# Kernel tuning notes

Measured on AMD Instinct MI355X. Metric: run time of the kernel, lower is better.

## Reference

```python
import jax, jax.numpy as jnp
import numpy as np

B, T, D = 128, 512, 300
U = 300          # gru_units
DENSE = 100      # dense_units
MASK_VALUE = 0.0


def setup_inputs() -> dict:
    key = jax.random.key(0)
    ks = jax.random.split(key, 8)
    s_in = 1.0 / np.sqrt(D)
    s_rec = 1.0 / np.sqrt(U)
    s_d = 1.0 / np.sqrt(2 * U)
    return {
        "x": jax.random.normal(ks[0], (B, T, D), jnp.float32),
        "Wf": jax.random.normal(ks[1], (D, 3 * U), jnp.float32) * s_in,
        "Uf": jax.random.normal(ks[2], (U, 3 * U), jnp.float32) * s_rec,
        "bf": jnp.zeros((2, 3 * U), jnp.float32),
        "Wb": jax.random.normal(ks[3], (D, 3 * U), jnp.float32) * s_in,
        "Ub": jax.random.normal(ks[4], (U, 3 * U), jnp.float32) * s_rec,
        "bb": jnp.zeros((2, 3 * U), jnp.float32),
        "Wd": jax.random.normal(ks[5], (2 * U, DENSE), jnp.float32) * s_d,
        "bd": jnp.zeros((DENSE,), jnp.float32),
    }


def _gru_dir(x, mask, W, Uw, b):
    """Keras GRU v2 (reset_after=True), one direction.
    x: [B,T,D], mask: [B,T] bool. Returns [B,T,U]."""
    # Precompute input projections for all timesteps (one big GEMM).
    xg = jnp.einsum('btd,dk->btk', x, W) + b[0]            # [B,T,3U]
    xg = jnp.swapaxes(xg, 0, 1)                             # [T,B,3U]
    m = jnp.swapaxes(mask, 0, 1)                            # [T,B]

    def step(h, inp):
        xt, mt = inp
        rec = h @ Uw + b[1]                                 # [B,3U]
        xz, xr, xh = jnp.split(xt, 3, axis=-1)
        rz, rr, rh = jnp.split(rec, 3, axis=-1)
        z = jax.nn.sigmoid(xz + rz)
        r = jax.nn.sigmoid(xr + rr)
        hh = jnp.tanh(xh + r * rh)
        h_new = z * h + (1.0 - z) * hh
        h_new = jnp.where(mt[:, None], h_new, h)            # masked: carry state
        return h_new, h_new

    h0 = jnp.zeros((x.shape[0], Uw.shape[0]), x.dtype)
    _, ys = jax.lax.scan(step, h0, (xg, m))
    return jnp.swapaxes(ys, 0, 1)                           # [B,T,U]


def reference(x, Wf, Uf, bf, Wb, Ub, bb, Wd, bd):
    # Masking layer: a timestep is masked if ALL features equal mask_value.
    mask = jnp.any(x != MASK_VALUE, axis=-1)                # [B,T]
    fwd = _gru_dir(x, mask, Wf, Uf, bf)
    bwd = _gru_dir(x[:, ::-1], mask[:, ::-1], Wb, Ub, bb)[:, ::-1]
    h = jnp.concatenate([fwd, bwd], axis=-1)                # [B,T,2U]
    # Dropout layers are identity at inference.
    out = jnp.tanh(jnp.einsum('btk,kd->btd', h, Wd) + bd)   # [B,T,DENSE]
    return out
```

## Files before the change

kernel.cpp:

```cpp
#include <hip/hip_runtime.h>


typedef float f32x4 __attribute__((ext_vector_type(4)));
typedef short short8 __attribute__((ext_vector_type(8)));
typedef unsigned short u16;
typedef unsigned int u32;
typedef unsigned long long u64;

#define MFMA16(a, b, c) __builtin_amdgcn_mfma_f32_16x16x32_bf16((a), (b), (c), 0, 0, 0)

__device__ __forceinline__ u16 f2bf(float f) {
  u32 u = __float_as_uint(f);
  u = u + 0x7FFFu + ((u >> 16) & 1u);
  return (u16)(u >> 16);
}
__device__ __forceinline__ float bf2f(u16 h) {
  return __uint_as_float(((u32)h) << 16);
}
__device__ __forceinline__ float sigm(float x) { return 1.f / (1.f + __expf(-x)); }
__device__ __forceinline__ float tanhx(float x) { return 1.f - 2.f / (__expf(2.f * x) + 1.f); }

#define OFF_WT       0ULL
#define OFF_UT       1228800ULL
#define OFF_B0P      2457600ULL
#define OFF_B1P      2465280ULL
#define OFF_WDT      2472960ULL
#define OFF_BDP      2616320ULL
#define OFF_MASK     2616832ULL
#define OFF_HSTATE   2878976ULL
#define OFF_FLAGS    3206656ULL
#define OFF_XBF      3223040ULL
#define OFF_HALL     45166080ULL
#define WS_NEED      123809280ULL

__global__ __launch_bounds__(256) void k_sentinel(float* __restrict__ out,
                                                  float code, int n) {
  int i = blockIdx.x * 256 + threadIdx.x;
  if (i < n) out[i] = code;
}

__global__ __launch_bounds__(256) void k_prep(
    const float* __restrict__ Wf, const float* __restrict__ Uf,
    const float* __restrict__ bfp, const float* __restrict__ Wb,
    const float* __restrict__ Ub, const float* __restrict__ bbp,
    const float* __restrict__ Wd, const float* __restrict__ bd,
    u16* __restrict__ WT, u16* __restrict__ UT,
    float* __restrict__ b0p, float* __restrict__ b1p,
    u16* __restrict__ WdT, float* __restrict__ bdp)
{
  const long long NWU = 2LL * 960 * 320;
  const long long TOTAL = NWU * 2 + 1920 + 71680 + 112;
  for (long long i = (long long)blockIdx.x * 256 + threadIdx.x; i < TOTAL;
       i += 2048LL * 256) {
    long long r = i;
    if (r < NWU) {
      int d = (int)(r / 307200); int q = (int)(r % 307200);
      int c = q / 320, k = q % 320;
      int cc = c / 80, lc = c % 80;
      float v = 0.f;
      if (k < 300 && lc < 75) {
        int g = lc / 25, jp = lc % 25;
        const float* W = d ? Wb : Wf;
        v = W[k * 900 + g * 300 + cc * 25 + jp];
      }
      WT[r] = f2bf(v);
      continue;
    }
    r -= NWU;
    if (r < NWU) {
      int d = (int)(r / 307200); int q = (int)(r % 307200);
      int c = q / 320, k = q % 320;
      int cc = c / 80, lc = c % 80;
      float v = 0.f;
      if (k < 300 && lc < 75) {
        int g = lc / 25, jp = lc % 25;
        const float* U = d ? Ub : Uf;
        v = U[k * 900 + g * 300 + cc * 25 + jp];
      }
      UT[r] = f2bf(v);
      continue;
    }
    r -= NWU;
    if (r < 1920) {
      int d = (int)(r / 960); int c = (int)(r % 960);
      int cc = c / 80, lc = c % 80;
      float v0 = 0.f, v1 = 0.f;
      if (lc < 75) {
        int g = lc / 25, jp = lc % 25;
        const float* B = d ? bbp : bfp;
        int sc = g * 300 + cc * 25 + jp;
        v0 = B[sc]; v1 = B[900 + sc];
      }
      b0p[r] = v0; b1p[r] = v1;
      continue;
    }
    r -= 1920;
    if (r < 71680) {
      int n = (int)(r / 640); int k = (int)(r % 640);
      float v = (n < 100 && k < 600) ? Wd[k * 100 + n] : 0.f;
      WdT[r] = f2bf(v);
      continue;
    }
    r -= 71680;
    if (r < 112) bdp[r] = (r < 100) ? bd[r] : 0.f;
  }
}

__global__ __launch_bounds__(256) void k_xbf(const float* __restrict__ x,
                                             u16* __restrict__ xbf,
                                             float* __restrict__ mask)
{
  int row = blockIdx.x * 4 + (threadIdx.x >> 6);
  int l = threadIdx.x & 63;
  const float* xr = x + (size_t)row * 300;
  u16* xo = xbf + (size_t)row * 320;
  int p = 0;
#pragma unroll
  for (int c = 0; c < 5; ++c) {
    int k = l + c * 64;
    float v = (k < 300) ? xr[k] : 0.f;
    p |= (v != 0.f);
    xo[k] = f2bf(v);
  }
  unsigned long long b = __ballot(p);
  if (l == 0) mask[row] = (b != 0ULL) ? 1.f : 0.f;
}

__global__ __launch_bounds__(256, 1) void k_scan(
    const u16* __restrict__ UTg, const u16* __restrict__ WTg,
    const float* __restrict__ b0p, const float* __restrict__ b1p,
    const u16* __restrict__ xbf, const float* __restrict__ mask,
    u16* __restrict__ h_state, u16* __restrict__ h_all, u32* __restrict__ flags)
{
  extern __shared__ char smem[];
  u16*   Ufrag = (u16*)smem;
  u16*   Wfrag = (u16*)(smem + 51200);
  char*  hS    = smem + 102400;
  float* recS  = (float*)(smem + 122880);
  float* xgS   = (float*)(smem + 133120);

  const int tid = threadIdx.x;
  const int l = tid & 63;
  const int w = tid >> 6;
  const bool is_x = (w >= 2);
  const int wm = w & 1;
  const int lc15 = l & 15, lq = l >> 4;

  const int bid = blockIdx.x;
  const int d = bid / 48;
  const int bc = (bid % 48) / 12;
  const int cc = bid % 12;

  {
    const u16* Ub = UTg + (size_t)(d * 12 + cc) * 80 * 320;
    const u16* Wb = WTg + (size_t)(d * 12 + cc) * 80 * 320;
    for (int u = tid; u < 3200; u += 256) {
      int fi = u >> 6, ll = u & 63;
      int nt = fi / 10, kt = fi % 10;
      int col = nt * 16 + (ll & 15);
      int k = kt * 32 + ((ll >> 4) << 3);
      *(uint4*)(Ufrag + (size_t)u * 8) = *(const uint4*)(Ub + (size_t)col * 320 + k);
      *(uint4*)(Wfrag + (size_t)u * 8) = *(const uint4*)(Wb + (size_t)col * 320 + k);
    }
  }

  float bv[5];
#pragma unroll
  for (int nt = 0; nt < 5; ++nt) {
    int col = d * 960 + cc * 80 + nt * 16 + lc15;
    bv[nt] = is_x ? b0p[col] : b1p[col];
  }

  int g_row[4], g_jp[4]; bool g_act[4];
#pragma unroll
  for (int it = 0; it < 4; ++it) {
    int i2 = tid + it * 256;
    g_act[it] = (i2 < 800);
    int rr = i2 / 25; if (rr > 31) rr = 31;
    g_row[it] = rr; g_jp[it] = i2 - (i2 / 25) * 25;
  }
  float hold[4];
#pragma unroll
  for (int it = 0; it < 4; ++it) hold[it] = 0.f;

  u16* hsA = h_state + (size_t)(d * 4 + bc) * 2 * 32 * 320;
  u32* flg = flags + (d * 4 + bc) * 512;

  __syncthreads();

  for (int t = 0; t < 512; ++t) {
    const int t_eff = d ? (511 - t) : t;

    short8 xF[10];
    if (is_x) {
      int row_b = bc * 32 + wm * 16 + lc15;
      const u16* xr = xbf + ((size_t)row_b * 512 + t_eff) * 320 + (lq << 3);
#pragma unroll
      for (int kt = 0; kt < 10; ++kt) xF[kt] = *(const short8*)(xr + kt * 32);
    }
    float mk[4];
#pragma unroll
    for (int it = 0; it < 4; ++it)
      mk[it] = g_act[it] ? mask[(size_t)(bc * 32 + g_row[it]) * 512 + t_eff] : 1.f;

    if (is_x) {
      f32x4 acc[5];
#pragma unroll
      for (int i = 0; i < 5; ++i) { f32x4 z = {0.f, 0.f, 0.f, 0.f}; acc[i] = z; }
#pragma unroll
      for (int kt = 0; kt < 10; ++kt) {
#pragma unroll
        for (int nt = 0; nt < 5; ++nt) {
          short8 bF = *(const short8*)(Wfrag + ((size_t)((nt * 10 + kt) * 64 + l)) * 8);
          acc[nt] = MFMA16(xF[kt], bF, acc[nt]);
        }
      }
#pragma unroll
      for (int nt = 0; nt < 5; ++nt) {
#pragma unroll
        for (int e = 0; e < 4; ++e)
          xgS[(wm * 16 + lq * 4 + e) * 80 + nt * 16 + lc15] = acc[nt][e] + bv[nt];
      }
    }

    if (t > 0 && tid == 0) {
      while (__hip_atomic_load(flg + (t - 1), __ATOMIC_ACQUIRE,
                               __HIP_MEMORY_SCOPE_AGENT) < 12u)
        __builtin_amdgcn_s_sleep(2);
    }
    __syncthreads();

    {
      const u16* hsrc = hsA + ((size_t)(t & 1)) * 32 * 320;
#pragma unroll
      for (int u0 = 0; u0 < 10; ++u0) {
        int u = tid + u0 * 256;
        int row = u / 80, c4 = u - (u / 80) * 80;
        u64 v = __hip_atomic_load((const u64*)(hsrc + (size_t)row * 320 + c4 * 4),
                                  __ATOMIC_RELAXED, __HIP_MEMORY_SCOPE_AGENT);
        *(u64*)(hS + row * 640 + ((c4 * 8) ^ ((row & 7) << 4))) = v;
      }
    }
    __syncthreads();

    if (!is_x) {
      const int r = wm * 16 + lc15;
      const int sw = (r & 7) << 4;
      const int rb = r * 640;
      f32x4 acc[5];
#pragma unroll
      for (int i = 0; i < 5; ++i) { f32x4 z = {0.f, 0.f, 0.f, 0.f}; acc[i] = z; }
#pragma unroll
      for (int kt = 0; kt < 10; ++kt) {
        short8 aF = *(const short8*)(hS + rb + ((kt * 64 + (lq << 4)) ^ sw));
#pragma unroll
        for (int nt = 0; nt < 5; ++nt) {
          short8 bF = *(const short8*)(Ufrag + ((size_t)((nt * 10 + kt) * 64 + l)) * 8);
          acc[nt] = MFMA16(aF, bF, acc[nt]);
        }
      }
#pragma unroll
      for (int nt = 0; nt < 5; ++nt) {
#pragma unroll
        for (int e = 0; e < 4; ++e)
          recS[(wm * 16 + lq * 4 + e) * 80 + nt * 16 + lc15] = acc[nt][e] + bv[nt];
      }
    }
    __syncthreads();

#pragma unroll
    for (int it = 0; it < 4; ++it) {
      if (g_act[it]) {
        int row = g_row[it], jp = g_jp[it];
        float xz = xgS[row * 80 + jp],      rz = recS[row * 80 + jp];
        float xr_ = xgS[row * 80 + 25 + jp], rr = recS[row * 80 + 25 + jp];
        float xh = xgS[row * 80 + 50 + jp],  rh = recS[row * 80 + 50 + jp];
        float z = sigm(xz + rz);
        float r = sigm(xr_ + rr);
        float hh = tanhx(xh + r * rh);
        float hn = z * hold[it] + (1.f - z) * hh;
        hn = (mk[it] != 0.f) ? hn : hold[it];
        hold[it] = hn;
        u16 hb = f2bf(hn);
        int jg = cc * 25 + jp;
        hsA[((size_t)((t + 1) & 1)) * 32 * 320 + (size_t)row * 320 + jg] = hb;
        size_t ridx = (size_t)(bc * 32 + row) * 512 + t_eff;
        h_all[ridx * 600 + d * 300 + jg] = hb;
      }
    }
    __syncthreads();
    if (tid == 0)
      __hip_atomic_fetch_add(flg + t, 1u, __ATOMIC_RELEASE, __HIP_MEMORY_SCOPE_AGENT);
  }
}

__global__ __launch_bounds__(256) void k_dense(
    const u16* __restrict__ h_all, const u16* __restrict__ WdT,
    const float* __restrict__ bdp, float* __restrict__ out)
{
  __shared__ u16 Bf[7 * 2 * 64 * 8];
  __shared__ char A[8192];
  const int tid = threadIdx.x;
  const int l = tid & 63;
  const int w = tid >> 6;
  const int lc15 = l & 15, lq = l >> 4;
  const int mblk = blockIdx.x;

  f32x4 acc[7];
#pragma unroll
  for (int i = 0; i < 7; ++i) { f32x4 z = {0.f, 0.f, 0.f, 0.f}; acc[i] = z; }

  for (int kc = 0; kc < 10; ++kc) {
    for (int u = tid; u < 512; u += 256) {
      int row = u >> 3, oct = u & 7;
      int k0 = kc * 64 + oct * 8;
      uint4 v = {0u, 0u, 0u, 0u};
      if (k0 <= 592)
        v = *(const uint4*)(h_all + (size_t)(mblk * 64 + row) * 600 + k0);
      *(uint4*)(A + row * 128 + ((oct * 16) ^ ((row & 7) << 4))) = v;
    }
    for (int u = tid; u < 896; u += 256) {
      int idx = u >> 6, ll = u & 63;
      int nt = idx >> 1, ktp = idx & 1;
      int kt = kc * 2 + ktp;
      uint4 v = {0u, 0u, 0u, 0u};
      if (kt < 19) {
        int col = nt * 16 + (ll & 15);
        int k = kt * 32 + ((ll >> 4) << 3);
        v = *(const uint4*)(WdT + (size_t)col * 640 + k);
      }
      *(uint4*)(Bf + (size_t)u * 8) = v;
    }
    __syncthreads();
    const int r = w * 16 + lc15;
    const int swA = (r & 7) << 4;
#pragma unroll
    for (int ktp = 0; ktp < 2; ++ktp) {
      if (kc * 2 + ktp < 19) {
        short8 aF = *(const short8*)(A + r * 128 + ((ktp * 64 + (lq << 4)) ^ swA));
#pragma unroll
        for (int nt = 0; nt < 7; ++nt) {
          short8 bF = *(const short8*)(Bf + ((size_t)((nt * 2 + ktp) * 64 + l)) * 8);
          acc[nt] = MFMA16(aF, bF, acc[nt]);
        }
      }
    }
    __syncthreads();
  }
#pragma unroll
  for (int nt = 0; nt < 7; ++nt) {
    int col = nt * 16 + lc15;
    if (col < 100) {
      float bb = bdp[col];
#pragma unroll
      for (int e = 0; e < 4; ++e) {
        int row = w * 16 + lq * 4 + e;
        out[(size_t)(mblk * 64 + row) * 100 + col] = tanhx(acc[nt][e] + bb);
      }
    }
  }
}

extern "C" void kernel_launch(void* const* d_in, const int* in_sizes, int n_in,
                              void* d_out, int out_size, void* d_ws, size_t ws_size,
                              hipStream_t stream)
{
  (void)in_sizes; (void)n_in;
  const float* x  = (const float*)d_in[0];
  const float* Wf = (const float*)d_in[1];
  const float* Uf = (const float*)d_in[2];
  const float* bf = (const float*)d_in[3];
  const float* Wb = (const float*)d_in[4];
  const float* Ub = (const float*)d_in[5];
  const float* bb = (const float*)d_in[6];
  const float* Wd = (const float*)d_in[7];
  const float* bd = (const float*)d_in[8];
  float* out = (float*)d_out;
  char* ws = (char*)d_ws;

  hipError_t e1 = hipFuncSetAttribute((const void*)k_scan,
      hipFuncAttributeMaxDynamicSharedMemorySize, 143360);

  if (ws_size < WS_NEED || e1 != hipSuccess) {
    float code = (float)(ws_size >> 20) + (e1 != hipSuccess ? 100000.f : 0.f);
    int n = out_size;
    hipLaunchKernelGGL(k_sentinel, dim3((n + 255) / 256), dim3(256), 0, stream,
                       out, code, n);
    return;
  }

  u16*   WT      = (u16*)(ws + OFF_WT);
  u16*   UT      = (u16*)(ws + OFF_UT);
  float* b0p     = (float*)(ws + OFF_B0P);
  float* b1p     = (float*)(ws + OFF_B1P);
  u16*   WdT     = (u16*)(ws + OFF_WDT);
  float* bdp     = (float*)(ws + OFF_BDP);
  float* mask    = (float*)(ws + OFF_MASK);
  u16*   h_state = (u16*)(ws + OFF_HSTATE);
  u32*   flags   = (u32*)(ws + OFF_FLAGS);
  u16*   xbf     = (u16*)(ws + OFF_XBF);
  u16*   h_all   = (u16*)(ws + OFF_HALL);

  hipMemsetAsync(ws + OFF_HSTATE, 0, 327680 + 16384, stream);

  hipLaunchKernelGGL(k_prep, dim3(2048), dim3(256), 0, stream,
                     Wf, Uf, bf, Wb, Ub, bb, Wd, bd, WT, UT, b0p, b1p, WdT, bdp);
  hipLaunchKernelGGL(k_xbf, dim3(16384), dim3(256), 0, stream, x, xbf, mask);
  hipLaunchKernelGGL(k_scan, dim3(96), dim3(256), 143360, stream,
                     UT, WT, b0p, b1p, xbf, mask, h_state, h_all, flags);
  hipLaunchKernelGGL(k_dense, dim3(1024), dim3(256), 0, stream,
                     h_all, WdT, bdp, out);
}
```

Measured before the change: 4.691 ms.

## Repartition GRU scan into 5 column chunks with per-chunk tags and register gates

The recurrent scan now runs on 40 blocks instead of 96. Each block owns 60 hidden units (192 padded columns, gate-interleaved) for 32 batch rows. The shared arrive counter is replaced by per-chunk monotonically increasing tags that each block polls from the other four chunks. Its own hidden slice stays in LDS, and the recurrent matmul's A operand is loaded straight from global into registers, which removes the LDS staging pass and a barrier. Gate math now reads the recurrent accumulators directly from MFMA registers, with the r/z biases folded into the input bias. The W projection streams from global/L2 instead of LDS. The risks are fewer CUs doing more MFMA work per step, and relaxed-ordering synchronisation that relies on an empty asm memory barrier.

After: 9.542 ms. 2.03x slower.

```diff
diff --git a/kernel.cpp b/kernel.cpp
--- a/kernel.cpp
+++ b/kernel.cpp
@@ -22,16 +22,16 @@
 
 #define OFF_WT       0ULL
 #define OFF_UT       1228800ULL
-#define OFF_B0P      2457600ULL
-#define OFF_B1P      2465280ULL
+#define OFF_BX       2457600ULL
+#define OFF_BH       2465280ULL
 #define OFF_WDT      2472960ULL
 #define OFF_BDP      2616320ULL
 #define OFF_MASK     2616832ULL
 #define OFF_HSTATE   2878976ULL
-#define OFF_FLAGS    3206656ULL
-#define OFF_XBF      3223040ULL
-#define OFF_HALL     45166080ULL
-#define WS_NEED      123809280ULL
+#define OFF_TAGS     3206656ULL
+#define OFF_XBF      3211776ULL
+#define OFF_HALL     45154816ULL
+#define WS_NEED      123798016ULL
 
 __global__ __launch_bounds__(256) void k_sentinel(float* __restrict__ out,
                                                   float code, int n) {
@@ -45,23 +45,24 @@
     const float* __restrict__ Ub, const float* __restrict__ bbp,
     const float* __restrict__ Wd, const float* __restrict__ bd,
     u16* __restrict__ WT, u16* __restrict__ UT,
-    float* __restrict__ b0p, float* __restrict__ b1p,
+    float* __restrict__ BX, float* __restrict__ BH,
     u16* __restrict__ WdT, float* __restrict__ bdp)
 {
-  const long long NWU = 2LL * 960 * 320;
-  const long long TOTAL = NWU * 2 + 1920 + 71680 + 112;
+  const long long NWU = 2LL * 5 * 192 * 320;
+  const long long TOTAL = NWU * 2 + 1920 * 2 + 71680 + 112;
   for (long long i = (long long)blockIdx.x * 256 + threadIdx.x; i < TOTAL;
        i += 2048LL * 256) {
     long long r = i;
     if (r < NWU) {
       int d = (int)(r / 307200); int q = (int)(r % 307200);
       int c = q / 320, k = q % 320;
-      int cc = c / 80, lc = c % 80;
+      int cc = c / 192, ccol = c % 192;
+      int tile = ccol / 16, ii = ccol % 16;
+      int m = tile / 3, g = tile % 3, jl = m * 16 + ii;
       float v = 0.f;
-      if (k < 300 && lc < 75) {
-        int g = lc / 25, jp = lc % 25;
+      if (k < 300 && jl < 60) {
         const float* W = d ? Wb : Wf;
-        v = W[k * 900 + g * 300 + cc * 25 + jp];
+        v = W[k * 900 + g * 300 + cc * 60 + jl];
       }
       WT[r] = f2bf(v);
       continue;
@@ -70,31 +71,36 @@
     if (r < NWU) {
       int d = (int)(r / 307200); int q = (int)(r % 307200);
       int c = q / 320, k = q % 320;
-      int cc = c / 80, lc = c % 80;
+      int cc = c / 192, ccol = c % 192;
+      int tile = ccol / 16, ii = ccol % 16;
+      int m = tile / 3, g = tile % 3, jl = m * 16 + ii;
+      int s = k / 64, jj = k % 64;
       float v = 0.f;
-      if (k < 300 && lc < 75) {
-        int g = lc / 25, jp = lc % 25;
+      if (jj < 60 && jl < 60) {
         const float* U = d ? Ub : Uf;
-        v = U[k * 900 + g * 300 + cc * 25 + jp];
+        v = U[(s * 60 + jj) * 900 + g * 300 + cc * 60 + jl];
       }
       UT[r] = f2bf(v);
       continue;
     }
     r -= NWU;
-    if (r < 1920) {
-      int d = (int)(r / 960); int c = (int)(r % 960);
-      int cc = c / 80, lc = c % 80;
-      float v0 = 0.f, v1 = 0.f;
-      if (lc < 75) {
-        int g = lc / 25, jp = lc % 25;
+    if (r < 1920 * 2) {
+      int which = (int)(r / 1920); int rr = (int)(r % 1920);
+      int d = rr / 960; int c = rr % 960;
+      int cc = c / 192, ccol = c % 192;
+      int tile = ccol / 16, ii = ccol % 16;
+      int m = tile / 3, g = tile % 3, jl = m * 16 + ii;
+      float v = 0.f;
+      if (jl < 60) {
         const float* B = d ? bbp : bfp;
-        int sc = g * 300 + cc * 25 + jp;
-        v0 = B[sc]; v1 = B[900 + sc];
-      }
-      b0p[r] = v0; b1p[r] = v1;
+        int col = g * 300 + cc * 60 + jl;
+        if (which == 0) v = B[col] + (g < 2 ? B[900 + col] : 0.f);
+        else            v = (g == 2) ? B[900 + col] : 0.f;
+      }
+      if (which == 0) BX[rr] = v; else BH[rr] = v;
       continue;
     }
-    r -= 1920;
+    r -= 1920 * 2;
     if (r < 71680) {
       int n = (int)(r / 640); int k = (int)(r % 640);
       float v = (n < 100 && k < 600) ? Wd[k * 100 + n] : 0.f;
@@ -128,169 +134,180 @@
 
 __global__ __launch_bounds__(256, 1) void k_scan(
     const u16* __restrict__ UTg, const u16* __restrict__ WTg,
-    const float* __restrict__ b0p, const float* __restrict__ b1p,
+    const float* __restrict__ BX, const float* __restrict__ BH,
     const u16* __restrict__ xbf, const float* __restrict__ mask,
-    u16* __restrict__ h_state, u16* __restrict__ h_all, u32* __restrict__ flags)
+    u16* __restrict__ h_state, u16* __restrict__ h_all, u32* __restrict__ tags)
 {
   extern __shared__ char smem[];
   u16*   Ufrag = (u16*)smem;
-  u16*   Wfrag = (u16*)(smem + 51200);
-  char*  hS    = smem + 102400;
-  float* recS  = (float*)(smem + 122880);
-  float* xgS   = (float*)(smem + 133120);
+  float* xgS   = (float*)(smem + 122880);
+  u16*   hOwn  = (u16*)(smem + 148992);
 
   const int tid = threadIdx.x;
   const int l = tid & 63;
   const int w = tid >> 6;
-  const bool is_x = (w >= 2);
-  const int wm = w & 1;
+  const bool isrec = (w < 2);
+  const int rt = isrec ? w : (w - 2);
   const int lc15 = l & 15, lq = l >> 4;
-
-  const int bid = blockIdx.x;
-  const int d = bid / 48;
-  const int bc = (bid % 48) / 12;
-  const int cc = bid % 12;
-
-  {
-    const u16* Ub = UTg + (size_t)(d * 12 + cc) * 80 * 320;
-    const u16* Wb = WTg + (size_t)(d * 12 + cc) * 80 * 320;
-    for (int u = tid; u < 3200; u += 256) {
-      int fi = u >> 6, ll = u & 63;
-      int nt = fi / 10, kt = fi % 10;
-      int col = nt * 16 + (ll & 15);
-      int k = kt * 32 + ((ll >> 4) << 3);
-      *(uint4*)(Ufrag + (size_t)u * 8) = *(const uint4*)(Ub + (size_t)col * 320 + k);
-      *(uint4*)(Wfrag + (size_t)u * 8) = *(const uint4*)(Wb + (size_t)col * 320 + k);
-    }
-  }
-
-  float bv[5];
-#pragma unroll
-  for (int nt = 0; nt < 5; ++nt) {
-    int col = d * 960 + cc * 80 + nt * 16 + lc15;
-    bv[nt] = is_x ? b0p[col] : b1p[col];
-  }
-
-  int g_row[4], g_jp[4]; bool g_act[4];
-#pragma unroll
-  for (int it = 0; it < 4; ++it) {
-    int i2 = tid + it * 256;
-    g_act[it] = (i2 < 800);
-    int rr = i2 / 25; if (rr > 31) rr = 31;
-    g_row[it] = rr; g_jp[it] = i2 - (i2 / 25) * 25;
-  }
-  float hold[4];
-#pragma unroll
-  for (int it = 0; it < 4; ++it) hold[it] = 0.f;
-
-  u16* hsA = h_state + (size_t)(d * 4 + bc) * 2 * 32 * 320;
-  u32* flg = flags + (d * 4 + bc) * 512;
+  const int row_loc = rt * 16 + lc15;
+
+  const int gb = blockIdx.x & 7;
+  const int cc = blockIdx.x >> 3;
+  const int d = gb >> 2, bc = gb & 3;
+
+  const size_t chunk = (size_t)(d * 5 + cc) * 192 * 320;
+  const u16* UT = UTg + chunk;
+  const u16* WT = WTg + chunk;
+
+  for (int u = tid; u < 7680; u += 256) {
+    int f = u >> 6, ll = u & 63;
+    int col = (f / 10) * 16 + (ll & 15);
+    int k = (f % 10) * 32 + ((ll >> 4) << 3);
+    *(uint4*)(Ufrag + (size_t)u * 8) = *(const uint4*)(UT + (size_t)col * 320 + k);
+  }
+  for (int u = tid; u < 1152; u += 256) ((u32*)hOwn)[u] = 0;
+
+  f32x4 bx[12]; f32x4 brh[4];
+  float hold[4][4];
+  if (isrec) {
+#pragma unroll
+    for (int m = 0; m < 4; ++m)
+      brh[m] = *(const f32x4*)(BH + d * 960 + cc * 192 + (3 * m + 2) * 16 + lq * 4);
+#pragma unroll
+    for (int m = 0; m < 4; ++m)
+#pragma unroll
+      for (int e = 0; e < 4; ++e) hold[m][e] = 0.f;
+  } else {
+#pragma unroll
+    for (int nt = 0; nt < 12; ++nt)
+      bx[nt] = *(const f32x4*)(BX + d * 960 + cc * 192 + nt * 16 + lq * 4);
+  }
+
+  const int growb = bc * 32 + row_loc;
+  u32* tg = tags + gb * 5 * 32;
+  const u16* wb = WT + (size_t)lc15 * 320 + (lq << 3);
 
   __syncthreads();
 
   for (int t = 0; t < 512; ++t) {
     const int t_eff = d ? (511 - t) : t;
-
-    short8 xF[10];
-    if (is_x) {
-      int row_b = bc * 32 + wm * 16 + lc15;
-      const u16* xr = xbf + ((size_t)row_b * 512 + t_eff) * 320 + (lq << 3);
+    const size_t ridx = (size_t)growb * 512 + t_eff;
+
+    f32x4 racc[12];
+    float mk = 1.f;
+
+    if (!isrec) {
+      short8 xF[10];
+      const u16* xr = xbf + ridx * 320 + (lq << 3);
 #pragma unroll
       for (int kt = 0; kt < 10; ++kt) xF[kt] = *(const short8*)(xr + kt * 32);
-    }
-    float mk[4];
-#pragma unroll
-    for (int it = 0; it < 4; ++it)
-      mk[it] = g_act[it] ? mask[(size_t)(bc * 32 + g_row[it]) * 512 + t_eff] : 1.f;
-
-    if (is_x) {
-      f32x4 acc[5];
-#pragma unroll
-      for (int i = 0; i < 5; ++i) { f32x4 z = {0.f, 0.f, 0.f, 0.f}; acc[i] = z; }
+#pragma unroll
+      for (int nt = 0; nt < 12; ++nt) { f32x4 z = {0.f, 0.f, 0.f, 0.f}; racc[nt] = z; }
 #pragma unroll
       for (int kt = 0; kt < 10; ++kt) {
 #pragma unroll
-        for (int nt = 0; nt < 5; ++nt) {
-          short8 bF = *(const short8*)(Wfrag + ((size_t)((nt * 10 + kt) * 64 + l)) * 8);
-          acc[nt] = MFMA16(xF[kt], bF, acc[nt]);
-        }
-      }
-#pragma unroll
-      for (int nt = 0; nt < 5; ++nt) {
-#pragma unroll
-        for (int e = 0; e < 4; ++e)
-          xgS[(wm * 16 + lq * 4 + e) * 80 + nt * 16 + lc15] = acc[nt][e] + bv[nt];
-      }
-    }
-
-    if (t > 0 && tid == 0) {
-      while (__hip_atomic_load(flg + (t - 1), __ATOMIC_ACQUIRE,
-                               __HIP_MEMORY_SCOPE_AGENT) < 12u)
-        __builtin_amdgcn_s_sleep(2);
-    }
+        for (int nt = 0; nt < 12; ++nt) {
+          short8 wf = *(const short8*)(wb + (size_t)nt * 5120 + kt * 32);
+          racc[nt] = MFMA16(wf, xF[kt], racc[nt]);
+        }
+      }
+#pragma unroll
+      for (int nt = 0; nt < 12; ++nt) {
+        f32x4 v = racc[nt] + bx[nt];
+        *(f32x4*)(xgS + row_loc * 204 + nt * 16 + lq * 4) = v;
+      }
+    } else {
+      mk = mask[ridx];
+      if (t > 0) {
+        u32 need = (u32)t;
+        for (;;) {
+          u32 mn = 0xffffffffu;
+#pragma unroll
+          for (int s = 0; s < 5; ++s) {
+            if (s != cc) {
+              u32 v = __hip_atomic_load(tg + s * 32, __ATOMIC_RELAXED,
+                                        __HIP_MEMORY_SCOPE_AGENT);
+              mn = v < mn ? v : mn;
+            }
+          }
+          if (mn >= need) break;
+          __builtin_amdgcn_s_sleep(1);
+        }
+        asm volatile("" ::: "memory");
+      }
+      short8 hf[10];
+      {
+        const int par = t & 1;
+        const u64* hb = (const u64*)(h_state +
+            (((size_t)(gb * 2 + par) * 32 + row_loc) * 5) * 64);
+#pragma unroll
+        for (int s = 0; s < 5; ++s) {
+          if (s == cc) continue;
+#pragma unroll
+          for (int kt2 = 0; kt2 < 2; ++kt2) {
+            const u64* p = hb + s * 16 + kt2 * 8 + lq * 2;
+            union { u64 q[2]; short8 v; } uu;
+            uu.q[0] = __hip_atomic_load(p, __ATOMIC_RELAXED, __HIP_MEMORY_SCOPE_AGENT);
+            uu.q[1] = __hip_atomic_load(p + 1, __ATOMIC_RELAXED, __HIP_MEMORY_SCOPE_AGENT);
+            hf[s * 2 + kt2] = uu.v;
+          }
+        }
+#pragma unroll
+        for (int kt2 = 0; kt2 < 2; ++kt2)
+          hf[cc * 2 + kt2] =
+              *(const short8*)(hOwn + row_loc * 72 + kt2 * 32 + (lq << 3));
+      }
+#pragma unroll
+      for (int nt = 0; nt < 12; ++nt) { f32x4 z = {0.f, 0.f, 0.f, 0.f}; racc[nt] = z; }
+#pragma unroll
+      for (int kt = 0; kt < 10; ++kt) {
+#pragma unroll
+        for (int nt = 0; nt < 12; ++nt) {
+          short8 uf = *(const short8*)(Ufrag + ((size_t)(nt * 10 + kt) * 64 + l) * 8);
+          racc[nt] = MFMA16(uf, hf[kt], racc[nt]);
+        }
+      }
+    }
+
     __syncthreads();
 
-    {
-      const u16* hsrc = hsA + ((size_t)(t & 1)) * 32 * 320;
-#pragma unroll
-      for (int u0 = 0; u0 < 10; ++u0) {
-        int u = tid + u0 * 256;
-        int row = u / 80, c4 = u - (u / 80) * 80;
-        u64 v = __hip_atomic_load((const u64*)(hsrc + (size_t)row * 320 + c4 * 4),
-                                  __ATOMIC_RELAXED, __HIP_MEMORY_SCOPE_AGENT);
-        *(u64*)(hS + row * 640 + ((c4 * 8) ^ ((row & 7) << 4))) = v;
-      }
-    }
-    __syncthreads();
-
-    if (!is_x) {
-      const int r = wm * 16 + lc15;
-      const int sw = (r & 7) << 4;
-      const int rb = r * 640;
-      f32x4 acc[5];
-#pragma unroll
-      for (int i = 0; i < 5; ++i) { f32x4 z = {0.f, 0.f, 0.f, 0.f}; acc[i] = z; }
-#pragma unroll
-      for (int kt = 0; kt < 10; ++kt) {
-        short8 aF = *(const short8*)(hS + rb + ((kt * 64 + (lq << 4)) ^ sw));
-#pragma unroll
-        for (int nt = 0; nt < 5; ++nt) {
-          short8 bF = *(const short8*)(Ufrag + ((size_t)((nt * 10 + kt) * 64 + l)) * 8);
-          acc[nt] = MFMA16(aF, bF, acc[nt]);
-        }
-      }
-#pragma unroll
-      for (int nt = 0; nt < 5; ++nt) {
-#pragma unroll
-        for (int e = 0; e < 4; ++e)
-          recS[(wm * 16 + lq * 4 + e) * 80 + nt * 16 + lc15] = acc[nt][e] + bv[nt];
-      }
-    }
-    __syncthreads();
-
-#pragma unroll
-    for (int it = 0; it < 4; ++it) {
-      if (g_act[it]) {
-        int row = g_row[it], jp = g_jp[it];
-        float xz = xgS[row * 80 + jp],      rz = recS[row * 80 + jp];
-        float xr_ = xgS[row * 80 + 25 + jp], rr = recS[row * 80 + 25 + jp];
-        float xh = xgS[row * 80 + 50 + jp],  rh = recS[row * 80 + 50 + jp];
-        float z = sigm(xz + rz);
-        float r = sigm(xr_ + rr);
-        float hh = tanhx(xh + r * rh);
-        float hn = z * hold[it] + (1.f - z) * hh;
-        hn = (mk[it] != 0.f) ? hn : hold[it];
-        hold[it] = hn;
-        u16 hb = f2bf(hn);
-        int jg = cc * 25 + jp;
-        hsA[((size_t)((t + 1) & 1)) * 32 * 320 + (size_t)row * 320 + jg] = hb;
-        size_t ridx = (size_t)(bc * 32 + row) * 512 + t_eff;
-        h_all[ridx * 600 + d * 300 + jg] = hb;
-      }
-    }
+    if (isrec) {
+      const float* xgr = xgS + row_loc * 204;
+      const bool msk = (mk != 0.f);
+#pragma unroll
+      for (int m = 0; m < 4; ++m) {
+        f32x4 xzv = *(const f32x4*)(xgr + (3 * m) * 16 + lq * 4);
+        f32x4 xrv = *(const f32x4*)(xgr + (3 * m + 1) * 16 + lq * 4);
+        f32x4 xhv = *(const f32x4*)(xgr + (3 * m + 2) * 16 + lq * 4);
+        u16 hb16[4];
+#pragma unroll
+        for (int e = 0; e < 4; ++e) {
+          float z = sigm(xzv[e] + racc[3 * m][e]);
+          float r = sigm(xrv[e] + racc[3 * m + 1][e]);
+          float hh = tanhx(xhv[e] + r * (racc[3 * m + 2][e] + brh[m][e]));
+          float hn = z * hold[m][e] + (1.f - z) * hh;
+          hn = msk ? hn : hold[m][e];
+          hold[m][e] = hn;
+          hb16[e] = f2bf(hn);
+        }
+        if (m < 3 || lq < 3) {
+          int j0 = m * 16 + lq * 4;
+          u32 lo = (u32)hb16[0] | ((u32)hb16[1] << 16);
+          u32 hi = (u32)hb16[2] | ((u32)hb16[3] << 16);
+          u64 pk = (u64)lo | ((u64)hi << 32);
+          u64* hp = (u64*)(h_state +
+              ((((size_t)(gb * 2 + ((t + 1) & 1)) * 32 + row_loc) * 5 + cc) * 64 + j0));
+          __hip_atomic_store(hp, pk, __ATOMIC_RELAXED, __HIP_MEMORY_SCOPE_AGENT);
+          *(u64*)(h_all + ridx * 600 + d * 300 + cc * 60 + j0) = pk;
+          *(u64*)(hOwn + row_loc * 72 + j0) = pk;
+        }
+      }
+    }
+
     __syncthreads();
     if (tid == 0)
-      __hip_atomic_fetch_add(flg + t, 1u, __ATOMIC_RELEASE, __HIP_MEMORY_SCOPE_AGENT);
+      __hip_atomic_store(tg + cc * 32, (u32)(t + 1), __ATOMIC_RELAXED,
+                         __HIP_MEMORY_SCOPE_AGENT);
   }
 }
 
@@ -379,7 +396,7 @@
   char* ws = (char*)d_ws;
 
   hipError_t e1 = hipFuncSetAttribute((const void*)k_scan,
-      hipFuncAttributeMaxDynamicSharedMemorySize, 143360);
+      hipFuncAttributeMaxDynamicSharedMemorySize, 153600);
 
   if (ws_size < WS_NEED || e1 != hipSuccess) {
     float code = (float)(ws_size >> 20) + (e1 != hipSuccess ? 100000.f : 0.f);
@@ -391,23 +408,23 @@
 
   u16*   WT      = (u16*)(ws + OFF_WT);
   u16*   UT      = (u16*)(ws + OFF_UT);
-  float* b0p     = (float*)(ws + OFF_B0P);
-  float* b1p     = (float*)(ws + OFF_B1P);
+  float* BX      = (float*)(ws + OFF_BX);
+  float* BH      = (float*)(ws + OFF_BH);
   u16*   WdT     = (u16*)(ws + OFF_WDT);
   float* bdp     = (float*)(ws + OFF_BDP);
   float* mask    = (float*)(ws + OFF_MASK);
   u16*   h_state = (u16*)(ws + OFF_HSTATE);
-  u32*   flags   = (u32*)(ws + OFF_FLAGS);
+  u32*   tags    = (u32*)(ws + OFF_TAGS);
   u16*   xbf     = (u16*)(ws + OFF_XBF);
   u16*   h_all   = (u16*)(ws + OFF_HALL);
 
-  hipMemsetAsync(ws + OFF_HSTATE, 0, 327680 + 16384, stream);
+  hipMemsetAsync(ws + OFF_HSTATE, 0, 327680 + 5120, stream);
 
   hipLaunchKernelGGL(k_prep, dim3(2048), dim3(256), 0, stream,
-                     Wf, Uf, bf, Wb, Ub, bb, Wd, bd, WT, UT, b0p, b1p, WdT, bdp);
+                     Wf, Uf, bf, Wb, Ub, bb, Wd, bd, WT, UT, BX, BH, WdT, bdp);
   hipLaunchKernelGGL(k_xbf, dim3(16384), dim3(256), 0, stream, x, xbf, mask);
-  hipLaunchKernelGGL(k_scan, dim3(96), dim3(256), 143360, stream,
-                     UT, WT, b0p, b1p, xbf, mask, h_state, h_all, flags);
+  hipLaunchKernelGGL(k_scan, dim3(40), dim3(256), 153600, stream,
+                     UT, WT, BX, BH, xbf, mask, h_state, h_all, tags);
   hipLaunchKernelGGL(k_dense, dim3(1024), dim3(256), 0, stream,
                      h_all, WdT, bdp, out);
 }
```
